# Kernel optimization log

Hardware: AMD Instinct MI355X
Metric: run time of the kernel (lower is better)

Reference implementation:

```python
import jax, jax.numpy as jnp
import numpy as np

N_NODES = 100000
N_EDGES = 1600000
F_IN = 128
HID = 64
HEADS = 2
N_CLASSES = 40
NEG_SLOPE = 0.2


def gat_conv(x, src, dst, W, a_src, a_dst, b, concat):
    # x: [N, F_in]; src/dst: [E] (self-loops already included)
    # W: [F_in, H*C]; a_src/a_dst: [H, C]; b: [H*C] or [C]
    N = x.shape[0]
    H, C = a_src.shape
    h = (x @ W).reshape(N, H, C)                      # [N, H, C]
    al_s = jnp.sum(h * a_src[None], axis=-1)          # [N, H]
    al_d = jnp.sum(h * a_dst[None], axis=-1)          # [N, H]
    e = jax.nn.leaky_relu(al_s[src] + al_d[dst], NEG_SLOPE)  # [E, H]
    # numerically-stable softmax over incoming edges of each dst node
    emax = jax.ops.segment_max(e, dst, num_segments=N)       # [N, H]
    ee = jnp.exp(e - emax[dst])
    denom = jax.ops.segment_sum(ee, dst, num_segments=N)     # [N, H]
    alpha = ee / (denom[dst] + 1e-16)                 # [E, H]
    msg = alpha[:, :, None] * h[src]                  # [E, H, C]
    out = jax.ops.segment_sum(msg, dst, num_segments=N)      # [N, H, C]
    out = out.reshape(N, H * C) if concat else out.mean(axis=1)
    return out + b


def setup_inputs() -> dict:
    key = jax.random.key(0)
    ks = jax.random.split(key, 9)
    s = 0.05
    x = jax.random.normal(ks[0], (N_NODES, F_IN), dtype=jnp.float32)
    edge_index = jax.random.randint(ks[1], (2, N_EDGES), 0, N_NODES, dtype=jnp.int32)
    W1 = jax.random.normal(ks[2], (F_IN, HEADS * HID), dtype=jnp.float32) * s
    a_src1 = jax.random.normal(ks[3], (HEADS, HID), dtype=jnp.float32) * s
    a_dst1 = jax.random.normal(ks[4], (HEADS, HID), dtype=jnp.float32) * s
    b1 = jnp.zeros((HEADS * HID,), dtype=jnp.float32)
    W2 = jax.random.normal(ks[5], (HEADS * HID, N_CLASSES), dtype=jnp.float32) * s
    a_src2 = jax.random.normal(ks[6], (1, N_CLASSES), dtype=jnp.float32) * s
    a_dst2 = jax.random.normal(ks[7], (1, N_CLASSES), dtype=jnp.float32) * s
    b2 = jnp.zeros((N_CLASSES,), dtype=jnp.float32)
    return {"x": x, "edge_index": edge_index, "W1": W1, "a_src1": a_src1,
            "a_dst1": a_dst1, "b1": b1, "W2": W2, "a_src2": a_src2,
            "a_dst2": a_dst2, "b2": b2}


def reference(x, edge_index, W1, a_src1, a_dst1, b1, W2, a_src2, a_dst2, b2):
    N = x.shape[0]
    loop = jnp.arange(N, dtype=edge_index.dtype)  # PyG GATConv adds self-loops
    src = jnp.concatenate([edge_index[0], loop])
    dst = jnp.concatenate([edge_index[1], loop])
    h = gat_conv(x, src, dst, W1, a_src1, a_dst1, b1, concat=True)   # [N, HEADS*HID]
    h = jax.nn.elu(h)                                                # activation (dropout p=0)
    h = gat_conv(h, src, dst, W2, a_src2, a_dst2, b2, concat=False)  # [N, N_CLASSES]
    return jax.nn.log_softmax(h, axis=1)
```

## Files before the change

### kernel.cpp

```cpp
#include <hip/hip_runtime.h>
#include <math.h>

#define NN   100000
#define NE   1600000
#define E2   (NE + NN)
#define NC   40
#define NEG  0.2f
#define MAXD 128

#define FMA4(acc_, s_, w_) { (acc_).x = fmaf((s_),(w_).x,(acc_).x); (acc_).y = fmaf((s_),(w_).y,(acc_).y); \
                             (acc_).z = fmaf((s_),(w_).z,(acc_).z); (acc_).w = fmaf((s_),(w_).w,(acc_).w); }

__device__ inline float b2f(unsigned short u) {
    union { unsigned int i; float f; } v; v.i = (unsigned int)u << 16; return v.f;
}
__device__ inline float4 b2f4(ushort4 u) {
    return make_float4(b2f(u.x), b2f(u.y), b2f(u.z), b2f(u.w));
}
__device__ inline unsigned short f2b(float f) {
    union { float f; unsigned int i; } v; v.f = f;
    unsigned int r = (v.i + 0x7FFFu + ((v.i >> 16) & 1u)) >> 16;
    return (unsigned short)r;
}
__device__ inline ushort4 f2b4(float4 f) {
    return make_ushort4(f2b(f.x), f2b(f.y), f2b(f.z), f2b(f.w));
}

__global__ __launch_bounds__(256) void gemm1_kernel(const float* __restrict__ x,
                                                    const float* __restrict__ W,
                                                    const float* __restrict__ a_s,
                                                    const float* __restrict__ a_d,
                                                    unsigned short* __restrict__ h1b,
                                                    float* __restrict__ als,
                                                    float* __restrict__ ald) {
    __shared__ float Ws[64 * 128];
    const float4* W4 = (const float4*)W;
    float4* Ws4 = (float4*)Ws;

    int cg = threadIdx.x & 31;
    int rg = threadIdx.x >> 5;
    int lane = threadIdx.x & 63;
    int row0 = blockIdx.x * 32 + rg * 4;
    const float4* x4 = (const float4*)x;

    float4 acc[4];
    acc[0] = acc[1] = acc[2] = acc[3] = make_float4(0.f, 0.f, 0.f, 0.f);

    for (int ph = 0; ph < 2; ++ph) {
        if (ph) __syncthreads();
        for (int i = threadIdx.x; i < 2048; i += 256) Ws4[i] = W4[ph * 2048 + i];
        __syncthreads();
        for (int k4 = 0; k4 < 16; ++k4) {
            float4 wv0 = Ws4[(k4 * 4 + 0) * 32 + cg];
            float4 wv1 = Ws4[(k4 * 4 + 1) * 32 + cg];
            float4 wv2 = Ws4[(k4 * 4 + 2) * 32 + cg];
            float4 wv3 = Ws4[(k4 * 4 + 3) * 32 + cg];
#pragma unroll
            for (int r = 0; r < 4; ++r) {
                float4 xv = x4[(row0 + r) * 32 + ph * 16 + k4];
                FMA4(acc[r], xv.x, wv0);
                FMA4(acc[r], xv.y, wv1);
                FMA4(acc[r], xv.z, wv2);
                FMA4(acc[r], xv.w, wv3);
            }
        }
    }
    ushort4* o4 = (ushort4*)h1b;
#pragma unroll
    for (int r = 0; r < 4; ++r) o4[(row0 + r) * 32 + cg] = f2b4(acc[r]);

    float4 asv = ((const float4*)a_s)[cg];
    float4 adv = ((const float4*)a_d)[cg];
#pragma unroll
    for (int r = 0; r < 4; ++r) {
        float ps = acc[r].x * asv.x + acc[r].y * asv.y + acc[r].z * asv.z + acc[r].w * asv.w;
        float pd = acc[r].x * adv.x + acc[r].y * adv.y + acc[r].z * adv.z + acc[r].w * adv.w;
#pragma unroll
        for (int mm = 1; mm <= 8; mm <<= 1) { ps += __shfl_xor(ps, mm); pd += __shfl_xor(pd, mm); }
        if ((lane & 15) == 0) {
            int h = cg >> 4;
            als[(row0 + r) * 2 + h] = ps;
            ald[(row0 + r) * 2 + h] = pd;
        }
    }
}

__global__ __launch_bounds__(256) void gemm2_kernel(const unsigned short* __restrict__ heluB,
                                                    const float* __restrict__ W,
                                                    unsigned short* __restrict__ h2b) {
    __shared__ float Ws[128 * 40];
    const float4* W4 = (const float4*)W;
    float4* Ws4 = (float4*)Ws;
    for (int i = threadIdx.x; i < 128 * 40 / 4; i += 256) Ws4[i] = W4[i];
    __syncthreads();

    int t = threadIdx.x;
    if (t >= 250) return;
    int cg = t % 10;
    int rg = t / 10;
    int row0 = blockIdx.x * 100 + rg * 4;
    const ushort4* x4 = (const ushort4*)heluB;

    float4 acc[4];
    acc[0] = acc[1] = acc[2] = acc[3] = make_float4(0.f, 0.f, 0.f, 0.f);

    for (int k4 = 0; k4 < 32; ++k4) {
        float4 wv0 = Ws4[(k4 * 4 + 0) * 10 + cg];
        float4 wv1 = Ws4[(k4 * 4 + 1) * 10 + cg];
        float4 wv2 = Ws4[(k4 * 4 + 2) * 10 + cg];
        float4 wv3 = Ws4[(k4 * 4 + 3) * 10 + cg];
#pragma unroll
        for (int r = 0; r < 4; ++r) {
            float4 xv = b2f4(x4[(row0 + r) * 32 + k4]);
            FMA4(acc[r], xv.x, wv0);
            FMA4(acc[r], xv.y, wv1);
            FMA4(acc[r], xv.z, wv2);
            FMA4(acc[r], xv.w, wv3);
        }
    }
    ushort4* o4 = (ushort4*)h2b;
#pragma unroll
    for (int r = 0; r < 4; ++r) o4[(row0 + r) * 10 + cg] = f2b4(acc[r]);
}

__global__ void cvec_kernel(const float* __restrict__ W2,
                            const float* __restrict__ a_s2,
                            const float* __restrict__ a_d2,
                            float* __restrict__ cs2,
                            float* __restrict__ cd2) {
    int k = threadIdx.x;
    float ss = 0.f, dd = 0.f;
    for (int c = 0; c < NC; ++c) {
        float wv = W2[k * NC + c];
        ss = fmaf(wv, a_s2[c], ss);
        dd = fmaf(wv, a_d2[c], dd);
    }
    cs2[k] = ss;
    cd2[k] = dd;
}

__global__ __launch_bounds__(256) void rank_kernel(const int* __restrict__ ei,
                                                   int* __restrict__ deg,
                                                   int* __restrict__ rank) {
    int j0 = (blockIdx.x * 256 + threadIdx.x) * 4;
    if (j0 >= E2) return;
    int4 r4;
    if (j0 < NE) {
        int4 d4 = *(const int4*)&ei[NE + j0];
        r4.x = atomicAdd(&deg[d4.x], 1);
        r4.y = atomicAdd(&deg[d4.y], 1);
        r4.z = atomicAdd(&deg[d4.z], 1);
        r4.w = atomicAdd(&deg[d4.w], 1);
    } else {
        int bse = j0 - NE;
        r4.x = atomicAdd(&deg[bse], 1);
        r4.y = atomicAdd(&deg[bse + 1], 1);
        r4.z = atomicAdd(&deg[bse + 2], 1);
        r4.w = atomicAdd(&deg[bse + 3], 1);
    }
    *(int4*)&rank[j0] = r4;
}

__global__ __launch_bounds__(256) void scan1_kernel(const int* __restrict__ deg,
                                                    int* __restrict__ offs,
                                                    int* __restrict__ bsum) {
    __shared__ int sh[256];
    int base = blockIdx.x * 1024 + threadIdx.x * 4;
    int v[4];
#pragma unroll
    for (int u = 0; u < 4; ++u) { int idx = base + u; v[u] = (idx < NN) ? deg[idx] : 0; }
    int t0 = v[0] + v[1] + v[2] + v[3];
    sh[threadIdx.x] = t0;
    __syncthreads();
    for (int off = 1; off < 256; off <<= 1) {
        int a = sh[threadIdx.x];
        int b = (threadIdx.x >= off) ? sh[threadIdx.x - off] : 0;
        __syncthreads();
        sh[threadIdx.x] = a + b;
        __syncthreads();
    }
    int excl = sh[threadIdx.x] - t0;
    if (threadIdx.x == 255) bsum[blockIdx.x] = sh[255];
    int run = excl;
#pragma unroll
    for (int u = 0; u < 4; ++u) { int idx = base + u; if (idx < NN) offs[idx] = run; run += v[u]; }
}

__global__ void scan2_kernel(int* __restrict__ bsum, int* __restrict__ offs) {
    __shared__ int sh[128];
    int i = threadIdx.x;
    int v = (i < 98) ? bsum[i] : 0;
    sh[i] = v;
    __syncthreads();
    for (int off = 1; off < 128; off <<= 1) {
        int a = sh[i];
        int b = (i >= off) ? sh[i - off] : 0;
        __syncthreads();
        sh[i] = a + b;
        __syncthreads();
    }
    if (i < 98) bsum[i] = sh[i] - v;
    if (i == 127) offs[NN] = sh[127];
}

__global__ __launch_bounds__(256) void scan3_kernel(int* __restrict__ offs,
                                                    const int* __restrict__ bsum) {
    int i = blockIdx.x * 256 + threadIdx.x;
    if (i < NN) offs[i] += bsum[i >> 10];
}

__global__ __launch_bounds__(256) void scatter_kernel(const int* __restrict__ ei,
                                                      const int* __restrict__ rank,
                                                      const int* __restrict__ offs,
                                                      int* __restrict__ csr) {
    int j0 = (blockIdx.x * 256 + threadIdx.x) * 4;
    if (j0 >= E2) return;
    int4 r4 = *(const int4*)&rank[j0];
    if (j0 < NE) {
        int4 s4 = *(const int4*)&ei[j0];
        int4 d4 = *(const int4*)&ei[NE + j0];
        csr[offs[d4.x] + r4.x] = s4.x;
        csr[offs[d4.y] + r4.y] = s4.y;
        csr[offs[d4.z] + r4.z] = s4.z;
        csr[offs[d4.w] + r4.w] = s4.w;
    } else {
        int bse = j0 - NE;
        csr[offs[bse] + r4.x]     = bse;
        csr[offs[bse + 1] + r4.y] = bse + 1;
        csr[offs[bse + 2] + r4.z] = bse + 2;
        csr[offs[bse + 3] + r4.w] = bse + 3;
    }
}

__global__ __launch_bounds__(256) void agg1_kernel(const int* __restrict__ offs,
                                                   const int* __restrict__ csr,
                                                   const float* __restrict__ als,
                                                   const float* __restrict__ ald,
                                                   const unsigned short* __restrict__ h1b,
                                                   const float* __restrict__ b,
                                                   const float* __restrict__ cs2,
                                                   const float* __restrict__ cd2,
                                                   unsigned short* __restrict__ heluB,
                                                   float* __restrict__ als2,
                                                   float* __restrict__ ald2) {
    __shared__ float wsh[4][2 * MAXD];
    __shared__ int   ssh[4][MAXD];
    int lane = threadIdx.x & 63;
    int nw = threadIdx.x >> 6;
    int node = blockIdx.x * 4 + nw;
    int start = offs[node], end = offs[node + 1];
    const float2* alsv = (const float2*)als;
    float2 adv = ((const float2*)ald)[node];
    float* wn = wsh[nw];
    int* sn = ssh[nw];

    float s0 = 0.f, s1 = 0.f;
    for (int j = start + lane; j < end; j += 64) {
        int idx = j - start;
        int s = csr[j];
        float2 a = alsv[s];
        float e0 = a.x + adv.x; e0 = e0 > 0.f ? e0 : NEG * e0;
        float e1 = a.y + adv.y; e1 = e1 > 0.f ? e1 : NEG * e1;
        float w0 = expf(e0), w1 = expf(e1);
        s0 += w0; s1 += w1;
        if (idx < MAXD) { wn[idx * 2] = w0; wn[idx * 2 + 1] = w1; sn[idx] = s; }
    }
    for (int mm = 32; mm; mm >>= 1) { s0 += __shfl_xor(s0, mm); s1 += __shfl_xor(s1, mm); }
    float inv0 = 1.f / (s0 + 1e-16f), inv1 = 1.f / (s1 + 1e-16f);

    int half = lane >> 5, l5 = lane & 31, hh = l5 >> 4;
    const ushort4* h14 = (const ushort4*)h1b;
    float4 acc = make_float4(0.f, 0.f, 0.f, 0.f);
    int j2 = start;
#define AGG1_FETCH(jv_, sv_, wv_) { \
        int idx_ = (jv_) - start; \
        if (idx_ < MAXD) { sv_ = sn[idx_]; wv_ = wn[idx_ * 2 + hh]; } \
        else { sv_ = csr[jv_]; float2 a_ = alsv[sv_]; \
               float e_ = (hh ? a_.y + adv.y : a_.x + adv.x); e_ = e_ > 0.f ? e_ : NEG * e_; wv_ = expf(e_); } }
    for (; j2 + 8 <= end; j2 += 8) {
        int jA = j2 + half, jB = jA + 2, jC = jA + 4, jD = jA + 6;
        int sA, sB, sC, sD; float wA, wB, wC, wD;
        AGG1_FETCH(jA, sA, wA); AGG1_FETCH(jB, sB, wB);
        AGG1_FETCH(jC, sC, wC); AGG1_FETCH(jD, sD, wD);
        float4 hA = b2f4(h14[sA * 32 + l5]);
        float4 hB = b2f4(h14[sB * 32 + l5]);
        float4 hC = b2f4(h14[sC * 32 + l5]);
        float4 hD = b2f4(h14[sD * 32 + l5]);
        FMA4(acc, wA, hA);
        FMA4(acc, wB, hB);
        FMA4(acc, wC, hC);
        FMA4(acc, wD, hD);
    }
    for (; j2 < end; j2 += 2) {
        int j = j2 + half;
        if (j < end) {
            int s; float w;
            AGG1_FETCH(j, s, w);
            float4 hv = b2f4(h14[s * 32 + l5]);
            FMA4(acc, w, hv);
        }
    }
#undef AGG1_FETCH
    acc.x += __shfl_xor(acc.x, 32); acc.y += __shfl_xor(acc.y, 32);
    acc.z += __shfl_xor(acc.z, 32); acc.w += __shfl_xor(acc.w, 32);
    if (lane < 32) {
        float inv = hh ? inv1 : inv0;
        float4 bb = ((const float4*)b)[l5];
        float4 o;
        o.x = fmaf(acc.x, inv, bb.x); o.y = fmaf(acc.y, inv, bb.y);
        o.z = fmaf(acc.z, inv, bb.z); o.w = fmaf(acc.w, inv, bb.w);
        o.x = o.x > 0.f ? o.x : expm1f(o.x); o.y = o.y > 0.f ? o.y : expm1f(o.y);
        o.z = o.z > 0.f ? o.z : expm1f(o.z); o.w = o.w > 0.f ? o.w : expm1f(o.w);
        ((ushort4*)heluB)[node * 32 + l5] = f2b4(o);

        float4 cs = ((const float4*)cs2)[l5];
        float4 cd = ((const float4*)cd2)[l5];
        float ps = o.x * cs.x + o.y * cs.y + o.z * cs.z + o.w * cs.w;
        float pd = o.x * cd.x + o.y * cd.y + o.z * cd.z + o.w * cd.w;
#pragma unroll
        for (int mm = 1; mm <= 16; mm <<= 1) { ps += __shfl_xor(ps, mm); pd += __shfl_xor(pd, mm); }
        if (l5 == 0) { als2[node] = ps; ald2[node] = pd; }
    }
}

__global__ __launch_bounds__(256) void agg2_kernel(const int* __restrict__ offs,
                                                   const int* __restrict__ csr,
                                                   const float* __restrict__ als,
                                                   const float* __restrict__ ald,
                                                   const unsigned short* __restrict__ h2b,
                                                   const float* __restrict__ b,
                                                   float* __restrict__ out) {
    __shared__ float  wsh[4][MAXD];
    __shared__ int    ssh[4][MAXD];
    __shared__ float4 red[4][6][10];
    int lane = threadIdx.x & 63;
    int nw = threadIdx.x >> 6;
    int node = blockIdx.x * 4 + nw;
    int start = offs[node], end = offs[node + 1];
    float ad = ald[node];
    float* wn = wsh[nw];
    int* sn = ssh[nw];

    float ssum = 0.f;
    for (int j = start + lane; j < end; j += 64) {
        int idx = j - start;
        int s = csr[j];
        float e = als[s] + ad; e = e > 0.f ? e : NEG * e;
        float w = expf(e);
        ssum += w;
        if (idx < MAXD) { wn[idx] = w; sn[idx] = s; }
    }
    for (int mm = 32; mm; mm >>= 1) ssum += __shfl_xor(ssum, mm);
    float inv = 1.f / (ssum + 1e-16f);

    int g = lane / 10, c = lane % 10;
    const ushort4* h24 = (const ushort4*)h2b;
#define AGG2_FETCH(jv_, sv_, wv_) { \
        int idx_ = (jv_) - start; \
        if (idx_ < MAXD) { sv_ = sn[idx_]; wv_ = wn[idx_]; } \
        else { sv_ = csr[jv_]; float e_ = als[sv_] + ad; e_ = e_ > 0.f ? e_ : NEG * e_; wv_ = expf(e_); } }
    if (g < 6) {
        float4 acc = make_float4(0.f, 0.f, 0.f, 0.f);
        int j2 = start;
        for (; j2 + 12 <= end; j2 += 12) {
            int jA = j2 + g, jB = jA + 6;
            int sA, sB; float wA, wB;
            AGG2_FETCH(jA, sA, wA); AGG2_FETCH(jB, sB, wB);
            float4 hA = b2f4(h24[sA * 10 + c]);
            float4 hB = b2f4(h24[sB * 10 + c]);
            FMA4(acc, wA, hA);
            FMA4(acc, wB, hB);
        }
        for (; j2 < end; j2 += 6) {
            int j = j2 + g;
            if (j < end) {
                int s; float w;
                AGG2_FETCH(j, s, w);
                float4 hv = b2f4(h24[s * 10 + c]);
                FMA4(acc, w, hv);
            }
        }
        red[nw][g][c] = acc;
    }
#undef AGG2_FETCH

    if (lane < 16) {
        bool act = lane < 10;
        float4 o = make_float4(-1e30f, -1e30f, -1e30f, -1e30f);
        if (act) {
            float4 tot = make_float4(0.f, 0.f, 0.f, 0.f);
#pragma unroll
            for (int k = 0; k < 6; ++k) {
                float4 r = red[nw][k][lane];
                tot.x += r.x; tot.y += r.y; tot.z += r.z; tot.w += r.w;
            }
            float4 bb = ((const float4*)b)[lane];
            o.x = fmaf(tot.x, inv, bb.x); o.y = fmaf(tot.y, inv, bb.y);
            o.z = fmaf(tot.z, inv, bb.z); o.w = fmaf(tot.w, inv, bb.w);
        }
        float mx = fmaxf(fmaxf(o.x, o.y), fmaxf(o.z, o.w));
#pragma unroll
        for (int mm = 1; mm <= 8; mm <<= 1) mx = fmaxf(mx, __shfl_xor(mx, mm));
        float es = (expf(o.x - mx) + expf(o.y - mx)) + (expf(o.z - mx) + expf(o.w - mx));
#pragma unroll
        for (int mm = 1; mm <= 8; mm <<= 1) es += __shfl_xor(es, mm);
        float lse = mx + logf(es);
        if (act) {
            float4 r;
            r.x = o.x - lse; r.y = o.y - lse; r.z = o.z - lse; r.w = o.w - lse;
            ((float4*)out)[node * 10 + lane] = r;
        }
    }
}

extern "C" void kernel_launch(void* const* d_in, const int* in_sizes, int n_in,
                              void* d_out, int out_size, void* d_ws, size_t ws_size,
                              hipStream_t stream) {
    const float* x   = (const float*)d_in[0];
    const int*   ei  = (const int*)  d_in[1];
    const float* W1  = (const float*)d_in[2];
    const float* as1 = (const float*)d_in[3];
    const float* ad1 = (const float*)d_in[4];
    const float* b1  = (const float*)d_in[5];
    const float* W2  = (const float*)d_in[6];
    const float* as2 = (const float*)d_in[7];
    const float* ad2 = (const float*)d_in[8];
    const float* b2  = (const float*)d_in[9];
    float* out = (float*)d_out;

    char* p = (char*)d_ws;
    auto alloc = [&](size_t bytes) { void* r = (void*)p; p += (bytes + 255) & ~size_t(255); return r; };
    unsigned short* h1b   = (unsigned short*)alloc(sizeof(unsigned short) * NN * 128);
    unsigned short* heluB = (unsigned short*)alloc(sizeof(unsigned short) * NN * 128);
    unsigned short* h2b   = (unsigned short*)alloc(sizeof(unsigned short) * NN * 40);
    float* als1 = (float*)alloc(sizeof(float) * NN * 2);
    float* ald1 = (float*)alloc(sizeof(float) * NN * 2);
    float* als2 = (float*)alloc(sizeof(float) * NN);
    float* ald2 = (float*)alloc(sizeof(float) * NN);
    float* cs2  = (float*)alloc(sizeof(float) * 128);
    float* cd2  = (float*)alloc(sizeof(float) * 128);
    int*   deg  = (int*)  alloc(sizeof(int) * NN);
    int*   offs = (int*)  alloc(sizeof(int) * (NN + 1));
    int*   bsum = (int*)  alloc(sizeof(int) * 128);
    int*   rank = (int*)  alloc(sizeof(int) * E2);
    int*   csr  = (int*)  alloc(sizeof(int) * E2);

    cvec_kernel<<<1, 128, 0, stream>>>(W2, as2, ad2, cs2, cd2);

    hipMemsetAsync(deg, 0, sizeof(int) * NN, stream);
    rank_kernel<<<(E2 / 4 + 255) / 256, 256, 0, stream>>>(ei, deg, rank);
    scan1_kernel<<<98, 256, 0, stream>>>(deg, offs, bsum);
    scan2_kernel<<<1, 128, 0, stream>>>(bsum, offs);
    scan3_kernel<<<(NN + 255) / 256, 256, 0, stream>>>(offs, bsum);
    scatter_kernel<<<(E2 / 4 + 255) / 256, 256, 0, stream>>>(ei, rank, offs, csr);

    gemm1_kernel<<<3125, 256, 0, stream>>>(x, W1, as1, ad1, h1b, als1, ald1);
    agg1_kernel<<<25000, 256, 0, stream>>>(offs, csr, als1, ald1, h1b, b1, cs2, cd2,
                                           heluB, als2, ald2);

    gemm2_kernel<<<1000, 256, 0, stream>>>(heluB, W2, h2b);
    agg2_kernel<<<25000, 256, 0, stream>>>(offs, csr, als2, ald2, h2b, b2, out);
}
```

Before: 435.4 us.

## Use bf16 MFMA with split-precision weights for both GAT GEMMs

Replaces the scalar FMA GEMMs for both layers with MFMA 16x16x32 bf16 instructions. Precision is kept close to fp32 by splitting operands into hi/lo bf16 parts: three MFMAs per tile in layer 1, two in layer 2. New prep kernels pre-split and swizzle the weights into an MFMA-friendly layout. The trade-off is extra MFMA work and the cost of converting x to bf16 pairs, and the h1b stores become scattered 2-byte writes.

```diff
diff --git a/kernel.cpp b/kernel.cpp
--- a/kernel.cpp
+++ b/kernel.cpp
@@ -11,6 +11,9 @@
 #define FMA4(acc_, s_, w_) { (acc_).x = fmaf((s_),(w_).x,(acc_).x); (acc_).y = fmaf((s_),(w_).y,(acc_).y); \
                              (acc_).z = fmaf((s_),(w_).z,(acc_).z); (acc_).w = fmaf((s_),(w_).w,(acc_).w); }
 
+typedef __attribute__((ext_vector_type(8))) short short8;
+typedef __attribute__((ext_vector_type(4))) float f32x4;
+
 __device__ inline float b2f(unsigned short u) {
     union { unsigned int i; float f; } v; v.i = (unsigned int)u << 16; return v.f;
 }
@@ -26,101 +29,147 @@
     return make_ushort4(f2b(f.x), f2b(f.y), f2b(f.z), f2b(f.w));
 }
 
-__global__ __launch_bounds__(256) void gemm1_kernel(const float* __restrict__ x,
-                                                    const float* __restrict__ W,
-                                                    const float* __restrict__ a_s,
-                                                    const float* __restrict__ a_d,
-                                                    unsigned short* __restrict__ h1b,
-                                                    float* __restrict__ als,
-                                                    float* __restrict__ ald) {
-    __shared__ float Ws[64 * 128];
-    const float4* W4 = (const float4*)W;
-    float4* Ws4 = (float4*)Ws;
-
-    int cg = threadIdx.x & 31;
-    int rg = threadIdx.x >> 5;
-    int lane = threadIdx.x & 63;
-    int row0 = blockIdx.x * 32 + rg * 4;
-    const float4* x4 = (const float4*)x;
-
-    float4 acc[4];
-    acc[0] = acc[1] = acc[2] = acc[3] = make_float4(0.f, 0.f, 0.f, 0.f);
-
-    for (int ph = 0; ph < 2; ++ph) {
-        if (ph) __syncthreads();
-        for (int i = threadIdx.x; i < 2048; i += 256) Ws4[i] = W4[ph * 2048 + i];
-        __syncthreads();
-        for (int k4 = 0; k4 < 16; ++k4) {
-            float4 wv0 = Ws4[(k4 * 4 + 0) * 32 + cg];
-            float4 wv1 = Ws4[(k4 * 4 + 1) * 32 + cg];
-            float4 wv2 = Ws4[(k4 * 4 + 2) * 32 + cg];
-            float4 wv3 = Ws4[(k4 * 4 + 3) * 32 + cg];
-#pragma unroll
-            for (int r = 0; r < 4; ++r) {
-                float4 xv = x4[(row0 + r) * 32 + ph * 16 + k4];
-                FMA4(acc[r], xv.x, wv0);
-                FMA4(acc[r], xv.y, wv1);
-                FMA4(acc[r], xv.z, wv2);
-                FMA4(acc[r], xv.w, wv3);
-            }
-        }
-    }
-    ushort4* o4 = (ushort4*)h1b;
-#pragma unroll
-    for (int r = 0; r < 4; ++r) o4[(row0 + r) * 32 + cg] = f2b4(acc[r]);
-
-    float4 asv = ((const float4*)a_s)[cg];
-    float4 adv = ((const float4*)a_d)[cg];
+__global__ void prep1_kernel(const float* __restrict__ W,
+                             unsigned short* __restrict__ wh,
+                             unsigned short* __restrict__ wl) {
+    int t = blockIdx.x * 256 + threadIdx.x;
+    int j = t & 7, lane = (t >> 3) & 63, ksnt = t >> 9;
+    int ks = ksnt & 3, nt = ksnt >> 2;
+    int k = ks * 32 + (lane >> 4) * 8 + j, col = nt * 16 + (lane & 15);
+    float w = W[k * 128 + col];
+    unsigned short h = f2b(w);
+    wh[t] = h; wl[t] = f2b(w - b2f(h));
+}
+
+__global__ void prep2_kernel(const float* __restrict__ W,
+                             unsigned short* __restrict__ wh,
+                             unsigned short* __restrict__ wl) {
+    int t = blockIdx.x * 256 + threadIdx.x;
+    int j = t & 7, lane = (t >> 3) & 63, ksnt = t >> 9;
+    int ks = ksnt & 3, nt = ksnt >> 2;
+    int k = ks * 32 + (lane >> 4) * 8 + j, col = nt * 16 + (lane & 15);
+    float w = (col < NC) ? W[k * NC + col] : 0.f;
+    unsigned short h = f2b(w);
+    wh[t] = h; wl[t] = f2b(w - b2f(h));
+}
+
+__global__ __launch_bounds__(256) void gemm1_mfma(const float* __restrict__ x,
+                                                  const unsigned short* __restrict__ wh,
+                                                  const unsigned short* __restrict__ wl,
+                                                  const float* __restrict__ a_s,
+                                                  const float* __restrict__ a_d,
+                                                  unsigned short* __restrict__ h1b,
+                                                  float* __restrict__ als,
+                                                  float* __restrict__ ald) {
+    __shared__ unsigned short whs[16384];
+    __shared__ unsigned short wls[16384];
+    {
+        const uint4* g1 = (const uint4*)wh; const uint4* g2 = (const uint4*)wl;
+        uint4* s1 = (uint4*)whs; uint4* s2 = (uint4*)wls;
+        for (int i = threadIdx.x; i < 2048; i += 256) { s1[i] = g1[i]; s2[i] = g2[i]; }
+    }
+    __syncthreads();
+    int wv = threadIdx.x >> 6, lane = threadIdx.x & 63;
+    int stripe = blockIdx.x * 4 + wv;
+    if (stripe >= 6250) return;
+    int row0 = stripe * 16;
+    int mrow = lane & 15, kg = lane >> 4;
+
+    f32x4 acc[8];
+#pragma unroll
+    for (int i = 0; i < 8; ++i) acc[i] = (f32x4){0.f, 0.f, 0.f, 0.f};
+
+    const float* xrow = x + (size_t)(row0 + mrow) * 128;
+    for (int ks = 0; ks < 4; ++ks) {
+        float4 v0 = *(const float4*)(xrow + ks * 32 + kg * 8);
+        float4 v1 = *(const float4*)(xrow + ks * 32 + kg * 8 + 4);
+        float vv[8] = {v0.x, v0.y, v0.z, v0.w, v1.x, v1.y, v1.z, v1.w};
+        short8 ah, alo;
+#pragma unroll
+        for (int j = 0; j < 8; ++j) {
+            unsigned short h = f2b(vv[j]);
+            ah[j]  = (short)h;
+            alo[j] = (short)f2b(vv[j] - b2f(h));
+        }
+#pragma unroll
+        for (int nt = 0; nt < 8; ++nt) {
+            short8 bh = *(const short8*)(whs + ((nt * 4 + ks) * 64 + lane) * 8);
+            short8 bl = *(const short8*)(wls + ((nt * 4 + ks) * 64 + lane) * 8);
+            acc[nt] = __builtin_amdgcn_mfma_f32_16x16x32_bf16(ah,  bh, acc[nt], 0, 0, 0);
+            acc[nt] = __builtin_amdgcn_mfma_f32_16x16x32_bf16(alo, bh, acc[nt], 0, 0, 0);
+            acc[nt] = __builtin_amdgcn_mfma_f32_16x16x32_bf16(ah,  bl, acc[nt], 0, 0, 0);
+        }
+    }
+
 #pragma unroll
     for (int r = 0; r < 4; ++r) {
-        float ps = acc[r].x * asv.x + acc[r].y * asv.y + acc[r].z * asv.z + acc[r].w * asv.w;
-        float pd = acc[r].x * adv.x + acc[r].y * adv.y + acc[r].z * adv.z + acc[r].w * adv.w;
-#pragma unroll
-        for (int mm = 1; mm <= 8; mm <<= 1) { ps += __shfl_xor(ps, mm); pd += __shfl_xor(pd, mm); }
-        if ((lane & 15) == 0) {
-            int h = cg >> 4;
-            als[(row0 + r) * 2 + h] = ps;
-            ald[(row0 + r) * 2 + h] = pd;
-        }
-    }
-}
-
-__global__ __launch_bounds__(256) void gemm2_kernel(const unsigned short* __restrict__ heluB,
-                                                    const float* __restrict__ W,
-                                                    unsigned short* __restrict__ h2b) {
-    __shared__ float Ws[128 * 40];
-    const float4* W4 = (const float4*)W;
-    float4* Ws4 = (float4*)Ws;
-    for (int i = threadIdx.x; i < 128 * 40 / 4; i += 256) Ws4[i] = W4[i];
+        int row = row0 + kg * 4 + r;
+#pragma unroll
+        for (int nt = 0; nt < 8; ++nt)
+            h1b[(size_t)row * 128 + nt * 16 + mrow] = f2b(acc[nt][r]);
+        float ps0 = 0.f, pd0 = 0.f, ps1 = 0.f, pd1 = 0.f;
+#pragma unroll
+        for (int nt = 0; nt < 4; ++nt) {
+            float av = a_s[nt * 16 + mrow], dv = a_d[nt * 16 + mrow];
+            ps0 = fmaf(acc[nt][r], av, ps0); pd0 = fmaf(acc[nt][r], dv, pd0);
+        }
+#pragma unroll
+        for (int nt = 4; nt < 8; ++nt) {
+            float av = a_s[nt * 16 + mrow], dv = a_d[nt * 16 + mrow];
+            ps1 = fmaf(acc[nt][r], av, ps1); pd1 = fmaf(acc[nt][r], dv, pd1);
+        }
+#pragma unroll
+        for (int mm = 1; mm <= 8; mm <<= 1) {
+            ps0 += __shfl_xor(ps0, mm); pd0 += __shfl_xor(pd0, mm);
+            ps1 += __shfl_xor(ps1, mm); pd1 += __shfl_xor(pd1, mm);
+        }
+        if (mrow == 0) {
+            als[row * 2]     = ps0; ald[row * 2]     = pd0;
+            als[row * 2 + 1] = ps1; ald[row * 2 + 1] = pd1;
+        }
+    }
+}
+
+__global__ __launch_bounds__(256) void gemm2_mfma(const unsigned short* __restrict__ heluB,
+                                                  const unsigned short* __restrict__ wh,
+                                                  const unsigned short* __restrict__ wl,
+                                                  unsigned short* __restrict__ h2b) {
+    __shared__ unsigned short whs[6144];
+    __shared__ unsigned short wls[6144];
+    {
+        const uint4* g1 = (const uint4*)wh; const uint4* g2 = (const uint4*)wl;
+        uint4* s1 = (uint4*)whs; uint4* s2 = (uint4*)wls;
+        for (int i = threadIdx.x; i < 768; i += 256) { s1[i] = g1[i]; s2[i] = g2[i]; }
+    }
     __syncthreads();
-
-    int t = threadIdx.x;
-    if (t >= 250) return;
-    int cg = t % 10;
-    int rg = t / 10;
-    int row0 = blockIdx.x * 100 + rg * 4;
-    const ushort4* x4 = (const ushort4*)heluB;
-
-    float4 acc[4];
-    acc[0] = acc[1] = acc[2] = acc[3] = make_float4(0.f, 0.f, 0.f, 0.f);
-
-    for (int k4 = 0; k4 < 32; ++k4) {
-        float4 wv0 = Ws4[(k4 * 4 + 0) * 10 + cg];
-        float4 wv1 = Ws4[(k4 * 4 + 1) * 10 + cg];
-        float4 wv2 = Ws4[(k4 * 4 + 2) * 10 + cg];
-        float4 wv3 = Ws4[(k4 * 4 + 3) * 10 + cg];
-#pragma unroll
-        for (int r = 0; r < 4; ++r) {
-            float4 xv = b2f4(x4[(row0 + r) * 32 + k4]);
-            FMA4(acc[r], xv.x, wv0);
-            FMA4(acc[r], xv.y, wv1);
-            FMA4(acc[r], xv.z, wv2);
-            FMA4(acc[r], xv.w, wv3);
-        }
-    }
-    ushort4* o4 = (ushort4*)h2b;
-#pragma unroll
-    for (int r = 0; r < 4; ++r) o4[(row0 + r) * 10 + cg] = f2b4(acc[r]);
+    int wv = threadIdx.x >> 6, lane = threadIdx.x & 63;
+    int stripe = blockIdx.x * 4 + wv;
+    if (stripe >= 6250) return;
+    int row0 = stripe * 16;
+    int mrow = lane & 15, kg = lane >> 4;
+
+    f32x4 acc[3];
+#pragma unroll
+    for (int i = 0; i < 3; ++i) acc[i] = (f32x4){0.f, 0.f, 0.f, 0.f};
+
+    const unsigned short* arow = heluB + (size_t)(row0 + mrow) * 128;
+    for (int ks = 0; ks < 4; ++ks) {
+        short8 a = *(const short8*)(arow + ks * 32 + kg * 8);
+#pragma unroll
+        for (int nt = 0; nt < 3; ++nt) {
+            short8 bh = *(const short8*)(whs + ((nt * 4 + ks) * 64 + lane) * 8);
+            short8 bl = *(const short8*)(wls + ((nt * 4 + ks) * 64 + lane) * 8);
+            acc[nt] = __builtin_amdgcn_mfma_f32_16x16x32_bf16(a, bh, acc[nt], 0, 0, 0);
+            acc[nt] = __builtin_amdgcn_mfma_f32_16x16x32_bf16(a, bl, acc[nt], 0, 0, 0);
+        }
+    }
+#pragma unroll
+    for (int r = 0; r < 4; ++r) {
+        int row = row0 + kg * 4 + r;
+        h2b[(size_t)row * 40 + mrow]      = f2b(acc[0][r]);
+        h2b[(size_t)row * 40 + 16 + mrow] = f2b(acc[1][r]);
+        if (mrow < 8) h2b[(size_t)row * 40 + 32 + mrow] = f2b(acc[2][r]);
+    }
 }
 
 __global__ void cvec_kernel(const float* __restrict__ W2,
@@ -439,6 +488,10 @@
     float* ald2 = (float*)alloc(sizeof(float) * NN);
     float* cs2  = (float*)alloc(sizeof(float) * 128);
     float* cd2  = (float*)alloc(sizeof(float) * 128);
+    unsigned short* wh1 = (unsigned short*)alloc(sizeof(unsigned short) * 16384);
+    unsigned short* wl1 = (unsigned short*)alloc(sizeof(unsigned short) * 16384);
+    unsigned short* wh2 = (unsigned short*)alloc(sizeof(unsigned short) * 6144);
+    unsigned short* wl2 = (unsigned short*)alloc(sizeof(unsigned short) * 6144);
     int*   deg  = (int*)  alloc(sizeof(int) * NN);
     int*   offs = (int*)  alloc(sizeof(int) * (NN + 1));
     int*   bsum = (int*)  alloc(sizeof(int) * 128);
@@ -446,18 +499,20 @@
     int*   csr  = (int*)  alloc(sizeof(int) * E2);
 
     cvec_kernel<<<1, 128, 0, stream>>>(W2, as2, ad2, cs2, cd2);
+    prep1_kernel<<<64, 256, 0, stream>>>(W1, wh1, wl1);
+    prep2_kernel<<<24, 256, 0, stream>>>(W2, wh2, wl2);
 
     hipMemsetAsync(deg, 0, sizeof(int) * NN, stream);
     rank_kernel<<<(E2 / 4 + 255) / 256, 256, 0, stream>>>(ei, deg, rank);
-    scan1_kernel<<<98, 256, 0, stream>>>(deg, offs, bsum);
+    scan1_kernel<<<98, 256, 0, stream>>>(bsum ? deg : deg, offs, bsum);
     scan2_kernel<<<1, 128, 0, stream>>>(bsum, offs);
     scan3_kernel<<<(NN + 255) / 256, 256, 0, stream>>>(offs, bsum);
     scatter_kernel<<<(E2 / 4 + 255) / 256, 256, 0, stream>>>(ei, rank, offs, csr);
 
-    gemm1_kernel<<<3125, 256, 0, stream>>>(x, W1, as1, ad1, h1b, als1, ald1);
+    gemm1_mfma<<<1563, 256, 0, stream>>>(x, wh1, wl1, as1, ad1, h1b, als1, ald1);
     agg1_kernel<<<25000, 256, 0, stream>>>(offs, csr, als1, ald1, h1b, b1, cs2, cd2,
                                            heluB, als2, ald2);
 
-    gemm2_kernel<<<1000, 256, 0, stream>>>(heluB, W2, h2b);
+    gemm2_mfma<<<1563, 256, 0, stream>>>(heluB, wh2, wl2, h2b);
     agg2_kernel<<<25000, 256, 0, stream>>>(offs, csr, als2, ald2, h2b, b2, out);
 }
```

Measured after the change: 383.7 us. -11.9%, faster.
